# Performance work log

Measured on AMD Instinct MI355X. Metric: run time of the kernel, lower is better.

## Reference

```python
import jax, jax.numpy as jnp
import numpy as np

CHANNELS = 256
HEADS = 8
GROUPS = 32
EPS = 1e-5


def setup_inputs() -> dict:
    key = jax.random.key(0)
    ks = jax.random.split(key, 9)
    c = CHANNELS
    s = 1.0 / np.sqrt(c)
    return {
        "x": jax.random.normal(ks[0], (2, c, 64, 64), dtype=jnp.float32),
        "gn_w": jnp.ones((c,), jnp.float32),
        "gn_b": jnp.zeros((c,), jnp.float32),
        "qkv_w": jax.random.normal(ks[1], (3 * c, c), jnp.float32) * s,
        "qkv_b": jnp.zeros((3 * c,), jnp.float32),
        "proj_w": jax.random.normal(ks[2], (c, c), jnp.float32) * s,
        "proj_b": jnp.zeros((c,), jnp.float32),
        "gproj_w": jax.random.normal(ks[3], (c, c), jnp.float32) * s,
        "gproj_b": jnp.zeros((c,), jnp.float32),
    }


def reference(x, gn_w, gn_b, qkv_w, qkv_b, proj_w, proj_b, gproj_w, gproj_b):
    b, c, h, w = x.shape
    n = h * w
    hd = c // HEADS
    scale = hd ** (-0.5)

    # GroupNorm(32, c)
    xg = x.reshape(b, GROUPS, -1)
    mu = jnp.mean(xg, axis=-1, keepdims=True)
    var = jnp.mean((xg - mu) ** 2, axis=-1, keepdims=True)
    xn = ((xg - mu) * jax.lax.rsqrt(var + EPS)).reshape(b, c, h, w)
    xn = xn * gn_w[None, :, None, None] + gn_b[None, :, None, None]

    # global context: AdaptiveAvgPool2d(1) + 1x1 conv -> [b, c]
    gfeat = jnp.mean(xn, axis=(2, 3))                      # [b, c]
    gfeat = gfeat @ gproj_w.T + gproj_b                    # [b, c]

    # qkv 1x1 conv
    qkv = jnp.einsum('bchw,oc->bohw', xn, qkv_w) + qkv_b[None, :, None, None]
    q, k, v = qkv[:, :c], qkv[:, c:2 * c], qkv[:, 2 * c:]

    q = q.reshape(b, HEADS, hd, n).transpose(0, 1, 3, 2)   # [b,H,N,d]
    k = k.reshape(b, HEADS, hd, n) + gfeat.reshape(b, HEADS, hd, 1) * 0.1  # [b,H,d,N]
    v = v.reshape(b, HEADS, hd, n).transpose(0, 1, 3, 2)   # [b,H,N,d]

    attn = jax.nn.softmax(jnp.einsum('bhnd,bhdm->bhnm', q, k) * scale, axis=-1)
    out = jnp.einsum('bhnm,bhmd->bhnd', attn, v)           # [b,H,N,d]
    out = out.transpose(0, 1, 3, 2).reshape(b, c, h, w)

    out = jnp.einsum('bchw,oc->bohw', out, proj_w) + proj_b[None, :, None, None]
    out = out + gfeat[:, :, None, None] * 0.1
    return out + x
```

## Files before the change

### kernel.cpp

```cpp
#include <hip/hip_runtime.h>
#include <hip/hip_bf16.h>
#include <stdint.h>

#define BATCH 2
#define CH 256
#define NSP 4096
#define HEADS 8
#define HD 32
#define GROUPS 32
#define EPS_GN 1e-5f
#define NSPLIT 4

#define ATT_SCALE (0.17677669529663687f * 1.4426950408889634f)

typedef __attribute__((ext_vector_type(8))) short short8;
typedef __attribute__((ext_vector_type(4))) float f32x4;
typedef __attribute__((ext_vector_type(16))) float f32x16;
typedef __attribute__((ext_vector_type(2))) float f32x2;

#define ZERO16 ((f32x16){0.f,0.f,0.f,0.f,0.f,0.f,0.f,0.f,0.f,0.f,0.f,0.f,0.f,0.f,0.f,0.f})

static __device__ __forceinline__ unsigned short f2bf(float f) {
    union { float f; unsigned u; } v; v.f = f;
    unsigned r = v.u + 0x7fffu + ((v.u >> 16) & 1u);
    return (unsigned short)(r >> 16);
}
static __device__ __forceinline__ unsigned pkbf(float x, float y) {
    __hip_bfloat162 h = __float22bfloat162_rn(make_float2(x, y));
    return *(unsigned*)&h;
}

__global__ void k_gnstats(const float* __restrict__ x, float* __restrict__ stats) {
    int bg = blockIdx.x;
    int t = threadIdx.x;
    const float4* b4 = (const float4*)(x + (size_t)bg * (8 * NSP));
    float s = 0.f, sq = 0.f;
    #pragma unroll
    for (int i = 0; i < 32; i++) {
        float4 v = b4[t + i * 256];
        s  += v.x + v.y + v.z + v.w;
        sq += v.x * v.x + v.y * v.y + v.z * v.z + v.w * v.w;
    }
    #pragma unroll
    for (int off = 32; off > 0; off >>= 1) {
        s  += __shfl_down(s, off);
        sq += __shfl_down(sq, off);
    }
    __shared__ float rs[4], rq[4];
    int w = t >> 6;
    if ((t & 63) == 0) { rs[w] = s; rq[w] = sq; }
    __syncthreads();
    if (t == 0) {
        float S = rs[0] + rs[1] + rs[2] + rs[3];
        float Q = rq[0] + rq[1] + rq[2] + rq[3];
        float mu  = S * (1.0f / 32768.0f);
        float var = Q * (1.0f / 32768.0f) - mu * mu;
        stats[bg * 2]     = mu;
        stats[bg * 2 + 1] = rsqrtf(var + EPS_GN);
    }
}

__global__ void k_gnapply(const float* __restrict__ x, const float* __restrict__ gn_w,
                          const float* __restrict__ gn_b, const float* __restrict__ stats,
                          unsigned short* __restrict__ xnt, float* __restrict__ gpart) {
    int p0 = blockIdx.x * 64, c0 = blockIdx.y * 64, b = blockIdx.z;
    int t = threadIdx.x;
    __shared__ float tile[64][65];
    int ci0 = t >> 4, pq = t & 15;
    #pragma unroll
    for (int k = 0; k < 4; k++) {
        int ci = ci0 + k * 16;
        int c = c0 + ci;
        float mu   = stats[(b * GROUPS + (c >> 3)) * 2];
        float rstd = stats[(b * GROUPS + (c >> 3)) * 2 + 1];
        float w  = gn_w[c] * rstd;
        float bb = gn_b[c] - mu * w;
        float4 v = *(const float4*)(x + ((size_t)(b * CH + c)) * NSP + p0 + pq * 4);
        tile[ci][pq * 4 + 0] = v.x * w + bb;
        tile[ci][pq * 4 + 1] = v.y * w + bb;
        tile[ci][pq * 4 + 2] = v.z * w + bb;
        tile[ci][pq * 4 + 3] = v.w * w + bb;
    }
    __syncthreads();
    int pi = t >> 2, cb = (t & 3) * 16;
    unsigned pack[8];
    #pragma unroll
    for (int e = 0; e < 8; e++) {
        float a  = tile[cb + 2 * e][pi];
        float bv = tile[cb + 2 * e + 1][pi];
        pack[e] = (unsigned)f2bf(a) | ((unsigned)f2bf(bv) << 16);
    }
    uint4* dst = (uint4*)(xnt + ((size_t)(b * NSP + p0 + pi)) * CH + c0 + cb);
    dst[0] = make_uint4(pack[0], pack[1], pack[2], pack[3]);
    dst[1] = make_uint4(pack[4], pack[5], pack[6], pack[7]);
    if (t < 64) {
        float s = 0.f;
        #pragma unroll
        for (int j = 0; j < 64; j++) s += tile[t][j];
        gpart[((size_t)(b * CH + c0 + t)) * 64 + blockIdx.x] = s;
    }
}

__global__ void k_gproj(const float* __restrict__ gpart, const float* __restrict__ gproj_w,
                        const float* __restrict__ gproj_b, float* __restrict__ gfeat) {
    int b = blockIdx.x, t = threadIdx.x;
    __shared__ float graw[256];
    const float* p = gpart + ((size_t)(b * CH + t)) * 64;
    float s = 0.f;
    #pragma unroll
    for (int i = 0; i < 64; i++) s += p[i];
    graw[t] = s * (1.0f / 4096.0f);
    __syncthreads();
    float acc = gproj_b[t];
    const float* wr = gproj_w + (size_t)t * CH;
    #pragma unroll 8
    for (int c = 0; c < 256; c++) acc += graw[c] * wr[c];
    gfeat[b * CH + t] = acc;
}

__global__ void k_convert(const float* __restrict__ qkv_w, const float* __restrict__ proj_w,
                          unsigned short* __restrict__ wbf) {
    int i4 = blockIdx.x * 256 + threadIdx.x;
    const float* src = (i4 < 49152) ? (qkv_w + (size_t)i4 * 4)
                                    : (proj_w + (size_t)(i4 - 49152) * 4);
    float4 v = *(const float4*)src;
    ushort4 o;
    o.x = f2bf(v.x); o.y = f2bf(v.y); o.z = f2bf(v.z); o.w = f2bf(v.w);
    *(ushort4*)(wbf + (size_t)i4 * 4) = o;
}

__global__ void k_gemm_qkv(const unsigned short* __restrict__ Ag,
                           const unsigned short* __restrict__ Btg,
                           const float* __restrict__ bias,
                           const float* __restrict__ gfeat,
                           unsigned short* __restrict__ qt,
                           unsigned short* __restrict__ kt,
                           unsigned short* __restrict__ vt) {
    int n0 = blockIdx.x * 128, m0 = blockIdx.y * 64, b = blockIdx.z;
    int t = threadIdx.x, lane = t & 63, w = t >> 6;
    int wm = w >> 1, wn = w & 1;
    __shared__ short A_lds[64][40];
    __shared__ short B_lds[128][40];
    const unsigned short* Bb = Btg + (size_t)b * NSP * CH;
    f32x4 acc[2][4];
    #pragma unroll
    for (int m = 0; m < 2; m++)
        #pragma unroll
        for (int n = 0; n < 4; n++) acc[m][n] = (f32x4){0.f, 0.f, 0.f, 0.f};
    int arow = t >> 2, akk = (t & 3) * 8;
    for (int k0 = 0; k0 < 256; k0 += 32) {
        __syncthreads();
        *(uint4*)&A_lds[arow][akk] = *(const uint4*)(Ag + (size_t)(m0 + arow) * CH + k0 + akk);
        #pragma unroll
        for (int hh = 0; hh < 2; hh++) {
            int f = t + hh * 256;
            int j = f >> 2, kk = (f & 3) * 8;
            *(uint4*)&B_lds[j][kk] = *(const uint4*)(Bb + (size_t)(n0 + j) * CH + k0 + kk);
        }
        __syncthreads();
        short8 a[2], bf[4];
        #pragma unroll
        for (int m = 0; m < 2; m++)
            a[m] = *(const short8*)&A_lds[wm * 32 + m * 16 + (lane & 15)][(lane >> 4) * 8];
        #pragma unroll
        for (int n = 0; n < 4; n++)
            bf[n] = *(const short8*)&B_lds[wn * 64 + n * 16 + (lane & 15)][(lane >> 4) * 8];
        #pragma unroll
        for (int m = 0; m < 2; m++)
            #pragma unroll
            for (int n = 0; n < 4; n++)
                acc[m][n] = __builtin_amdgcn_mfma_f32_16x16x32_bf16(a[m], bf[n], acc[m][n], 0, 0, 0);
    }
    int rbase = m0 + wm * 32 + ((lane >> 4) << 2);
    int cbase = n0 + wn * 64 + (lane & 15);
    #pragma unroll
    for (int m = 0; m < 2; m++) {
        int row0 = rbase + m * 16;
        int sec = row0 >> 8;
        int ch  = row0 & 255;
        int h = ch >> 5, d0 = ch & 31;
        #pragma unroll
        for (int n = 0; n < 4; n++) {
            int col = cbase + n * 16;
            if (sec == 0) {
                ushort4 pk;
                pk.x = f2bf(acc[m][n][0] + bias[row0 + 0]);
                pk.y = f2bf(acc[m][n][1] + bias[row0 + 1]);
                pk.z = f2bf(acc[m][n][2] + bias[row0 + 2]);
                pk.w = f2bf(acc[m][n][3] + bias[row0 + 3]);
                *(ushort4*)(qt + ((size_t)((b * 8 + h) * NSP + col)) * HD + d0) = pk;
            } else if (sec == 1) {
                ushort4 pk;
                #pragma unroll
                for (int i = 0; i < 4; i++) {
                    float v = (acc[m][n][i] + bias[row0 + i]
                               + 0.1f * gfeat[b * CH + ch + i]) * ATT_SCALE;
                    ((unsigned short*)&pk)[i] = f2bf(v);
                }
                *(ushort4*)(kt + ((size_t)((b * 8 + h) * NSP + col)) * HD + d0) = pk;
            } else {
                #pragma unroll
                for (int i = 0; i < 4; i++) {
                    float v = acc[m][n][i] + bias[row0 + i];
                    vt[((size_t)((b * 8 + h) * HD + d0 + i)) * NSP + col] = f2bf(v);
                }
            }
        }
    }
}

__global__ void k_gemm_proj(const unsigned short* __restrict__ Ag,
                            const unsigned short* __restrict__ Btg,
                            const float* __restrict__ bias,
                            const float* __restrict__ gfeat,
                            const float* __restrict__ xres,
                            float* __restrict__ out) {
    int n0 = blockIdx.x * 128, m0 = blockIdx.y * 64, b = blockIdx.z;
    int t = threadIdx.x, lane = t & 63, w = t >> 6;
    int wm = w >> 1, wn = w & 1;
    __shared__ short A_lds[64][40];
    __shared__ short B_lds[128][40];
    const unsigned short* Bb = Btg + (size_t)b * NSP * CH;
    f32x4 acc[2][4];
    #pragma unroll
    for (int m = 0; m < 2; m++)
        #pragma unroll
        for (int n = 0; n < 4; n++) acc[m][n] = (f32x4){0.f, 0.f, 0.f, 0.f};
    int arow = t >> 2, akk = (t & 3) * 8;
    for (int k0 = 0; k0 < 256; k0 += 32) {
        __syncthreads();
        *(uint4*)&A_lds[arow][akk] = *(const uint4*)(Ag + (size_t)(m0 + arow) * CH + k0 + akk);
        #pragma unroll
        for (int hh = 0; hh < 2; hh++) {
            int f = t + hh * 256;
            int j = f >> 2, kk = (f & 3) * 8;
            *(uint4*)&B_lds[j][kk] = *(const uint4*)(Bb + (size_t)(n0 + j) * CH + k0 + kk);
        }
        __syncthreads();
        short8 a[2], bf[4];
        #pragma unroll
        for (int m = 0; m < 2; m++)
            a[m] = *(const short8*)&A_lds[wm * 32 + m * 16 + (lane & 15)][(lane >> 4) * 8];
        #pragma unroll
        for (int n = 0; n < 4; n++)
            bf[n] = *(const short8*)&B_lds[wn * 64 + n * 16 + (lane & 15)][(lane >> 4) * 8];
        #pragma unroll
        for (int m = 0; m < 2; m++)
            #pragma unroll
            for (int n = 0; n < 4; n++)
                acc[m][n] = __builtin_amdgcn_mfma_f32_16x16x32_bf16(a[m], bf[n], acc[m][n], 0, 0, 0);
    }
    int rbase = m0 + wm * 32 + ((lane >> 4) << 2);
    int cbase = n0 + wn * 64 + (lane & 15);
    #pragma unroll
    for (int m = 0; m < 2; m++) {
        #pragma unroll
        for (int n = 0; n < 4; n++) {
            int col = cbase + n * 16;
            #pragma unroll
            for (int i = 0; i < 4; i++) {
                int row = rbase + m * 16 + i;
                float add = bias[row] + 0.1f * gfeat[b * CH + row]
                          + xres[((size_t)(b * CH + row)) * NSP + col];
                out[((size_t)(b * CH + row)) * NSP + col] = acc[m][n][i] + add;
            }
        }
    }
}

__global__ __launch_bounds__(256)
void k_flash32(const unsigned short* __restrict__ qt,
               const unsigned short* __restrict__ kt,
               const unsigned short* __restrict__ vt,
               unsigned short* __restrict__ opart, float* __restrict__ lmpart) {
    const int h = blockIdx.y, b = blockIdx.z;
    const int s = blockIdx.x >> 5;
    const int t = threadIdx.x, lane = t & 63, w = t >> 6;
    const int lo32 = lane & 31, hi = lane >> 5;
    const int q0 = (blockIdx.x & 31) * 128 + w * 32;
    const int j0base = s * (NSP / NSPLIT);
    const unsigned short* qp = qt + ((size_t)(b * 8 + h) * NSP) * HD;
    const unsigned short* kp = kt + ((size_t)(b * 8 + h) * NSP) * HD;
    const unsigned short* vp = vt + ((size_t)(b * 8 + h) * HD) * NSP;
    __shared__ __align__(16) unsigned short K_lds[64 * 40];
    __shared__ __align__(16) unsigned short V_lds[32 * 64];

    short8 qf0 = *(const short8*)(qp + (size_t)(q0 + lo32) * HD + hi * 8);
    short8 qf1 = *(const short8*)(qp + (size_t)(q0 + lo32) * HD + 16 + hi * 8);
    f32x16 oacc;
    #pragma unroll
    for (int i = 0; i < 16; i++) oacc[i] = 0.f;
    float m = -1e30f, l = 0.f;

    const int krow = (t & 7) + 8 * (t >> 5);
    const int kslot = (t >> 3) & 3;
    const int vd = t >> 3, vslot = t & 7;
    const unsigned short* kga = kp + (size_t)(j0base + krow) * HD + kslot * 8;
    const unsigned short* vga = vp + (size_t)vd * NSP + j0base + vslot * 8;
    uint4 kreg = *(const uint4*)kga;
    uint4 vreg = *(const uint4*)vga;
    const int kws = krow * 40 + kslot * 8;
    const int vws = vd * 64 + ((vslot ^ (vd & 7)) * 8);

    const int NT = NSP / NSPLIT / 64;
    for (int it = 0; it < NT; ++it) {
        *(uint4*)&K_lds[kws] = kreg;
        *(uint4*)&V_lds[vws] = vreg;
        __syncthreads();
        if (it + 1 < NT) {
            kreg = *(const uint4*)(kga + (size_t)(it + 1) * 64 * HD);
            vreg = *(const uint4*)(vga + (it + 1) * 64);
        }
        const int jA = lo32, jB = 32 + lo32;
        short8 k00 = *(const short8*)&K_lds[jA * 40 + hi * 8];
        short8 k01 = *(const short8*)&K_lds[jA * 40 + (2 + hi) * 8];
        short8 k10 = *(const short8*)&K_lds[jB * 40 + hi * 8];
        short8 k11 = *(const short8*)&K_lds[jB * 40 + (2 + hi) * 8];
        f32x16 sv0, sv1;
        __builtin_amdgcn_s_setprio(1);
        sv0 = __builtin_amdgcn_mfma_f32_32x32x16_bf16(k00, qf0, ZERO16, 0, 0, 0);
        sv0 = __builtin_amdgcn_mfma_f32_32x32x16_bf16(k01, qf1, sv0, 0, 0, 0);
        sv1 = __builtin_amdgcn_mfma_f32_32x32x16_bf16(k10, qf0, ZERO16, 0, 0, 0);
        sv1 = __builtin_amdgcn_mfma_f32_32x32x16_bf16(k11, qf1, sv1, 0, 0, 0);
        __builtin_amdgcn_s_setprio(0);
        float h0 = fmaxf(fmaxf(sv0[0],  sv0[1]),  sv0[2]);
        float h1 = fmaxf(fmaxf(sv0[3],  sv0[4]),  sv0[5]);
        float h2 = fmaxf(fmaxf(sv0[6],  sv0[7]),  sv0[8]);
        float h3 = fmaxf(fmaxf(sv0[9],  sv0[10]), sv0[11]);
        float h4 = fmaxf(fmaxf(sv0[12], sv0[13]), sv0[14]);
        float h5 = fmaxf(fmaxf(sv1[0],  sv1[1]),  sv1[2]);
        float h6 = fmaxf(fmaxf(sv1[3],  sv1[4]),  sv1[5]);
        float h7 = fmaxf(fmaxf(sv1[6],  sv1[7]),  sv1[8]);
        float h8 = fmaxf(fmaxf(sv1[9],  sv1[10]), sv1[11]);
        float h9 = fmaxf(fmaxf(sv1[12], sv1[13]), sv1[14]);
        float r0 = fmaxf(fmaxf(h0, h1), h2);
        float r1 = fmaxf(fmaxf(h3, h4), h5);
        float r2 = fmaxf(fmaxf(h6, h7), h8);
        float r3 = fmaxf(fmaxf(h9, sv0[15]), sv1[15]);
        float vmx = fmaxf(fmaxf(r0, r1), fmaxf(r2, r3));
        vmx = fmaxf(vmx, __shfl_xor(vmx, 32));
        if (__any(vmx > m + 8.f)) {
            float nm = fmaxf(m, vmx);
            float corr = __builtin_amdgcn_exp2f(m - nm);
            m = nm;
            l *= corr;
            #pragma unroll
            for (int i = 0; i < 16; i++) oacc[i] *= corr;
        }
        #pragma unroll
        for (int i = 0; i < 16; i++) {
            sv0[i] = __builtin_amdgcn_exp2f(sv0[i] - m);
            sv1[i] = __builtin_amdgcn_exp2f(sv1[i] - m);
        }
        {
            #define SH2(V, I) __builtin_shufflevector(V, V, 2*(I), 2*(I)+1)
            f32x2 t0 = (SH2(sv0,0) + SH2(sv0,1)) + (SH2(sv0,2) + SH2(sv0,3));
            f32x2 t1 = (SH2(sv0,4) + SH2(sv0,5)) + (SH2(sv0,6) + SH2(sv0,7));
            f32x2 t2 = (SH2(sv1,0) + SH2(sv1,1)) + (SH2(sv1,2) + SH2(sv1,3));
            f32x2 t3 = (SH2(sv1,4) + SH2(sv1,5)) + (SH2(sv1,6) + SH2(sv1,7));
            f32x2 tt = (t0 + t1) + (t2 + t3);
            float sm = tt[0] + tt[1];
            #undef SH2
            sm += __shfl_xor(sm, 32);
            l += sm;
        }
        #define PVSTEP(SV, BB, C) { \
            unsigned p0 = pkbf(SV[BB + 0], SV[BB + 1]); \
            unsigned p1 = pkbf(SV[BB + 2], SV[BB + 3]); \
            unsigned p2 = pkbf(SV[BB + 4], SV[BB + 5]); \
            unsigned p3 = pkbf(SV[BB + 6], SV[BB + 7]); \
            unsigned s0 = hi ? p0 : p2, s1 = hi ? p1 : p3; \
            unsigned r0 = __shfl_xor(s0, 32), r1 = __shfl_xor(s1, 32); \
            uint4 fu = hi ? make_uint4(r0, r1, p2, p3) : make_uint4(p0, p1, r0, r1); \
            short8 pa = *(short8*)&fu; \
            short8 vf = *(const short8*)&V_lds[lo32 * 64 + ((((C) * 2 + hi) ^ (lo32 & 7)) * 8)]; \
            oacc = __builtin_amdgcn_mfma_f32_32x32x16_bf16(vf, pa, oacc, 0, 0, 0); \
        }
        __builtin_amdgcn_s_setprio(1);
        PVSTEP(sv0, 0, 0)
        PVSTEP(sv0, 8, 1)
        PVSTEP(sv1, 0, 2)
        PVSTEP(sv1, 8, 3)
        __builtin_amdgcn_s_setprio(0);
        #undef PVSTEP
        __syncthreads();
    }
    unsigned short* op = opart + ((((size_t)s * BATCH + b) * HEADS + h) * NSP + q0 + lo32) * HD;
    #pragma unroll
    for (int rr = 0; rr < 4; rr++) {
        ushort4 pk4;
        pk4.x = f2bf(oacc[rr * 4 + 0]);
        pk4.y = f2bf(oacc[rr * 4 + 1]);
        pk4.z = f2bf(oacc[rr * 4 + 2]);
        pk4.w = f2bf(oacc[rr * 4 + 3]);
        *(ushort4*)(op + rr * 8 + hi * 4) = pk4;
    }
    if (hi == 0)
        *(float2*)(lmpart + ((((size_t)s * BATCH + b) * HEADS + h) * NSP + q0 + lo32) * 2)
            = make_float2(m, l);
}

__global__ __launch_bounds__(256)
void k_combine(const unsigned short* __restrict__ opart, const float* __restrict__ lmpart,
               unsigned short* __restrict__ att) {
    int flat = blockIdx.x * 256 + threadIdx.x;
    int dchunk = flat & 3;
    int q = (flat >> 2) & (NSP - 1);
    int bh = flat >> 14;
    const size_t sO = (size_t)BATCH * HEADS * NSP * HD;
    const size_t sL = (size_t)BATCH * HEADS * NSP * 2;
    size_t rowq = (size_t)bh * NSP + q;
    float2 lm[NSPLIT];
    float M = -1e30f;
    #pragma unroll
    for (int s2 = 0; s2 < NSPLIT; s2++) {
        lm[s2] = *(const float2*)(lmpart + s2 * sL + rowq * 2);
        M = fmaxf(M, lm[s2].x);
    }
    float den = 0.f, cw[NSPLIT];
    #pragma unroll
    for (int s2 = 0; s2 < NSPLIT; s2++) {
        cw[s2] = __builtin_amdgcn_exp2f(lm[s2].x - M);
        den += lm[s2].y * cw[s2];
    }
    float inv = 1.0f / den;
    float acc[8];
    #pragma unroll
    for (int e = 0; e < 8; e++) acc[e] = 0.f;
    #pragma unroll
    for (int s2 = 0; s2 < NSPLIT; s2++) {
        uint4 v = *(const uint4*)(opart + s2 * sO + rowq * HD + dchunk * 8);
        float wgt = cw[s2] * inv;
        const unsigned short* pv = (const unsigned short*)&v;
        #pragma unroll
        for (int e = 0; e < 8; e++) {
            unsigned u = (unsigned)pv[e] << 16;
            acc[e] += wgt * *(float*)&u;
        }
    }
    uint4 o;
    o.x = (unsigned)f2bf(acc[0]) | ((unsigned)f2bf(acc[1]) << 16);
    o.y = (unsigned)f2bf(acc[2]) | ((unsigned)f2bf(acc[3]) << 16);
    o.z = (unsigned)f2bf(acc[4]) | ((unsigned)f2bf(acc[5]) << 16);
    o.w = (unsigned)f2bf(acc[6]) | ((unsigned)f2bf(acc[7]) << 16);
    *(uint4*)(att + ((size_t)((bh >> 3) * NSP + q)) * CH + (bh & 7) * HD + dchunk * 8) = o;
}

extern "C" void kernel_launch(void* const* d_in, const int* in_sizes, int n_in,
                              void* d_out, int out_size, void* d_ws, size_t ws_size,
                              hipStream_t stream) {
    const float* x       = (const float*)d_in[0];
    const float* gn_w    = (const float*)d_in[1];
    const float* gn_b    = (const float*)d_in[2];
    const float* qkv_w   = (const float*)d_in[3];
    const float* qkv_b   = (const float*)d_in[4];
    const float* proj_w  = (const float*)d_in[5];
    const float* proj_b  = (const float*)d_in[6];
    const float* gproj_w = (const float*)d_in[7];
    const float* gproj_b = (const float*)d_in[8];
    char* ws = (char*)d_ws;
    float*          stats  = (float*)(ws);
    float*          gpart  = (float*)(ws + 1024);
    float*          gfeat  = (float*)(ws + 132096);
    unsigned short* wbf    = (unsigned short*)(ws + 134144);
    unsigned short* xnt    = (unsigned short*)(ws + 658432);
    float*          lmpart = (float*)(ws + 658432);
    unsigned short* qt     = (unsigned short*)(ws + 4852736);
    unsigned short* kt     = (unsigned short*)(ws + 9047040);
    unsigned short* vt     = (unsigned short*)(ws + 13241344);
    unsigned short* att    = (unsigned short*)(ws + 17435648);
    unsigned short* opart  = (unsigned short*)(ws + 21629952);
    float* out = (float*)d_out;

    hipLaunchKernelGGL(k_gnstats, dim3(64), dim3(256), 0, stream, x, stats);
    hipLaunchKernelGGL(k_gnapply, dim3(64, 4, 2), dim3(256), 0, stream,
                       x, gn_w, gn_b, stats, xnt, gpart);
    hipLaunchKernelGGL(k_gproj, dim3(2), dim3(256), 0, stream,
                       gpart, gproj_w, gproj_b, gfeat);
    hipLaunchKernelGGL(k_convert, dim3(256), dim3(256), 0, stream, qkv_w, proj_w, wbf);
    hipLaunchKernelGGL(k_gemm_qkv, dim3(32, 12, 2), dim3(256), 0, stream,
                       wbf, xnt, qkv_b, gfeat, qt, kt, vt);
    hipLaunchKernelGGL(k_flash32, dim3(32 * NSPLIT, 8, 2), dim3(256), 0, stream,
                       qt, kt, vt, opart, lmpart);
    hipLaunchKernelGGL(k_combine, dim3(1024), dim3(256), 0, stream,
                       opart, lmpart, att);
    hipLaunchKernelGGL(k_gemm_proj, dim3(32, 4, 2), dim3(256), 0, stream,
                       wbf + 196608, att, proj_b, gfeat, x, out);
}
```

Baseline: 126.9 us.

## Double-buffer K/V shared-memory tiles in flash attention, one barrier per iteration

The K and V tiles in LDS become double buffers. Each iteration writes the next tile into the alternate buffer while computing on the current one, and the second __syncthreads per iteration is removed. Global prefetch now runs two tiles ahead. The max subtraction and rescale are also written as vector operations, which is mostly cosmetic. The change doubles LDS use (about 18KB per block), which could limit occupancy.

Result: no change. 129.4 us (+2.0%).

```diff
diff --git a/kernel.cpp b/kernel.cpp
--- a/kernel.cpp
+++ b/kernel.cpp
@@ -282,8 +282,8 @@
     const unsigned short* qp = qt + ((size_t)(b * 8 + h) * NSP) * HD;
     const unsigned short* kp = kt + ((size_t)(b * 8 + h) * NSP) * HD;
     const unsigned short* vp = vt + ((size_t)(b * 8 + h) * HD) * NSP;
-    __shared__ __align__(16) unsigned short K_lds[64 * 40];
-    __shared__ __align__(16) unsigned short V_lds[32 * 64];
+    __shared__ __align__(16) unsigned short K_lds[2][64 * 40];
+    __shared__ __align__(16) unsigned short V_lds[2][32 * 64];
 
     short8 qf0 = *(const short8*)(qp + (size_t)(q0 + lo32) * HD + hi * 8);
     short8 qf1 = *(const short8*)(qp + (size_t)(q0 + lo32) * HD + 16 + hi * 8);
@@ -297,25 +297,35 @@
     const int vd = t >> 3, vslot = t & 7;
     const unsigned short* kga = kp + (size_t)(j0base + krow) * HD + kslot * 8;
     const unsigned short* vga = vp + (size_t)vd * NSP + j0base + vslot * 8;
+    const int kws = krow * 40 + kslot * 8;
+    const int vws = vd * 64 + ((vslot ^ (vd & 7)) * 8);
+
+    const int NT = NSP / NSPLIT / 64;
     uint4 kreg = *(const uint4*)kga;
     uint4 vreg = *(const uint4*)vga;
-    const int kws = krow * 40 + kslot * 8;
-    const int vws = vd * 64 + ((vslot ^ (vd & 7)) * 8);
-
-    const int NT = NSP / NSPLIT / 64;
+    *(uint4*)&K_lds[0][kws] = kreg;
+    *(uint4*)&V_lds[0][vws] = vreg;
+    kreg = *(const uint4*)(kga + (size_t)64 * HD);
+    vreg = *(const uint4*)(vga + 64);
+
     for (int it = 0; it < NT; ++it) {
-        *(uint4*)&K_lds[kws] = kreg;
-        *(uint4*)&V_lds[vws] = vreg;
+        const int cur = it & 1;
         __syncthreads();
         if (it + 1 < NT) {
-            kreg = *(const uint4*)(kga + (size_t)(it + 1) * 64 * HD);
-            vreg = *(const uint4*)(vga + (it + 1) * 64);
-        }
+            *(uint4*)&K_lds[cur ^ 1][kws] = kreg;
+            *(uint4*)&V_lds[cur ^ 1][vws] = vreg;
+        }
+        if (it + 2 < NT) {
+            kreg = *(const uint4*)(kga + (size_t)(it + 2) * 64 * HD);
+            vreg = *(const uint4*)(vga + (it + 2) * 64);
+        }
+        const unsigned short* Kb = &K_lds[cur][0];
+        const unsigned short* Vb = &V_lds[cur][0];
         const int jA = lo32, jB = 32 + lo32;
-        short8 k00 = *(const short8*)&K_lds[jA * 40 + hi * 8];
-        short8 k01 = *(const short8*)&K_lds[jA * 40 + (2 + hi) * 8];
-        short8 k10 = *(const short8*)&K_lds[jB * 40 + hi * 8];
-        short8 k11 = *(const short8*)&K_lds[jB * 40 + (2 + hi) * 8];
+        short8 k00 = *(const short8*)&Kb[jA * 40 + hi * 8];
+        short8 k01 = *(const short8*)&Kb[jA * 40 + (2 + hi) * 8];
+        short8 k10 = *(const short8*)&Kb[jB * 40 + hi * 8];
+        short8 k11 = *(const short8*)&Kb[jB * 40 + (2 + hi) * 8];
         f32x16 sv0, sv1;
         __builtin_amdgcn_s_setprio(1);
         sv0 = __builtin_amdgcn_mfma_f32_32x32x16_bf16(k00, qf0, ZERO16, 0, 0, 0);
@@ -344,13 +354,14 @@
             float corr = __builtin_amdgcn_exp2f(m - nm);
             m = nm;
             l *= corr;
-            #pragma unroll
-            for (int i = 0; i < 16; i++) oacc[i] *= corr;
-        }
+            oacc *= corr;
+        }
+        sv0 -= m;
+        sv1 -= m;
         #pragma unroll
         for (int i = 0; i < 16; i++) {
-            sv0[i] = __builtin_amdgcn_exp2f(sv0[i] - m);
-            sv1[i] = __builtin_amdgcn_exp2f(sv1[i] - m);
+            sv0[i] = __builtin_amdgcn_exp2f(sv0[i]);
+            sv1[i] = __builtin_amdgcn_exp2f(sv1[i]);
         }
         {
             #define SH2(V, I) __builtin_shufflevector(V, V, 2*(I), 2*(I)+1)
@@ -373,7 +384,7 @@
             unsigned r0 = __shfl_xor(s0, 32), r1 = __shfl_xor(s1, 32); \
             uint4 fu = hi ? make_uint4(r0, r1, p2, p3) : make_uint4(p0, p1, r0, r1); \
             short8 pa = *(short8*)&fu; \
-            short8 vf = *(const short8*)&V_lds[lo32 * 64 + ((((C) * 2 + hi) ^ (lo32 & 7)) * 8)]; \
+            short8 vf = *(const short8*)&Vb[lo32 * 64 + ((((C) * 2 + hi) ^ (lo32 & 7)) * 8)]; \
             oacc = __builtin_amdgcn_mfma_f32_32x32x16_bf16(vf, pa, oacc, 0, 0, 0); \
         }
         __builtin_amdgcn_s_setprio(1);
@@ -383,7 +394,6 @@
         PVSTEP(sv1, 8, 3)
         __builtin_amdgcn_s_setprio(0);
         #undef PVSTEP
-        __syncthreads();
     }
     unsigned short* op = opart + ((((size_t)s * BATCH + b) * HEADS + h) * NSP + q0 + lo32) * HD;
     #pragma unroll
```
